# Performance work log

Measured on AMD Instinct MI355X. Metric: run time of the kernel, lower is better.

The kernel has to match this reference:

```python
import jax, jax.numpy as jnp
import numpy as np

HEADS = 8

def setup_inputs() -> dict:
    key = jax.random.key(0)
    ks = jax.random.split(key, 10)
    B, S, E = 2, 2048, 512
    q = jax.random.normal(ks[0], (B, S, E), jnp.float32)
    k = jax.random.normal(ks[1], (B, S, E), jnp.float32)
    v = jax.random.normal(ks[2], (B, S, E), jnp.float32)
    mask = jnp.zeros((S, S), jnp.float32)  # additive mask [s_q, s_k]
    scale = 0.02
    Wq = jax.random.normal(ks[3], (E, E), jnp.float32) * scale
    bq = jax.random.normal(ks[4], (E,), jnp.float32) * scale
    Wk = jax.random.normal(ks[5], (E, E), jnp.float32) * scale
    bk = jax.random.normal(ks[6], (E,), jnp.float32) * scale
    Wv = jax.random.normal(ks[7], (E, E), jnp.float32) * scale
    bv = jax.random.normal(ks[8], (E,), jnp.float32) * scale
    return {"q": q, "k": k, "v": v, "mask": mask,
            "Wq": Wq, "bq": bq, "Wk": Wk, "bk": bk, "Wv": Wv, "bv": bv}

def reference(q, k, v, mask, Wq, bq, Wk, bk, Wv, bv):
    H = HEADS
    b, s_q, _ = q.shape
    s_k = k.shape[1]
    s_v = v.shape[1]
    # NOTE: faithful to source: row-major view(b, H, s, -1) WITHOUT transposing
    # seq/head axes first (quirk of the original module).
    K = jnp.swapaxes((k @ Wk.T + bk).reshape(b, H, s_k, -1), 2, 3)  # [b,H,dh,s_k]
    Q = (q @ Wq.T + bq).reshape(b, H, s_q, -1)                      # [b,H,s_q,dh]
    V = (v @ Wv.T + bv).reshape(b, H, s_v, -1)                      # [b,H,s_v,dh]
    # NOTE: original scales by sqrt(K.shape[-1]) AFTER the transpose, i.e. sqrt(s_k)
    scores = (Q @ K) / jnp.sqrt(jnp.asarray(s_k, jnp.float32))      # [b,H,s_q,s_k]
    scores = scores + mask[:s_q, :s_k]
    attn = jax.nn.softmax(scores, axis=-1)
    out = (attn @ V).reshape(b, s_q, -1)  # [b, s_q, e]
    return out
```

## Files before the change

kernel.cpp:

```cpp
#include <hip/hip_runtime.h>


#define SEQ 2048
#define EMB 512
#define DH  64
#define MROWS 4096
#define NROWS 32768

typedef float  v4f __attribute__((ext_vector_type(4)));
typedef short  v8s __attribute__((ext_vector_type(8)));
typedef __fp16 v2h __attribute__((ext_vector_type(2)));

static __device__ __forceinline__ unsigned int f2bf(float f) {
    unsigned int u = __float_as_uint(f);
    u += 0x7fffu + ((u >> 16) & 1u);
    return u >> 16;
}
static __device__ __forceinline__ unsigned int pack2(float a, float b) {
    return f2bf(a) | (f2bf(b) << 16);
}
static __device__ __forceinline__ unsigned int packh2(float a, float b) {
    v2h h = __builtin_amdgcn_cvt_pkrtz(a, b);
    return __builtin_bit_cast(unsigned int, h);
}

__global__ __launch_bounds__(256, 3) void proj_kernel(
    const float* __restrict__ q, const float* __restrict__ k, const float* __restrict__ v,
    const float* __restrict__ Wq, const float* __restrict__ bq,
    const float* __restrict__ Wk, const float* __restrict__ bk,
    const float* __restrict__ Wv, const float* __restrict__ bv,
    const float* __restrict__ mask,
    unsigned short* __restrict__ Qbf, unsigned short* __restrict__ Kbf,
    unsigned short* __restrict__ Vbf, float* __restrict__ maskT,
    unsigned int* __restrict__ flags)
{
    __shared__ __align__(16) char smem[27648];
    const int tid = threadIdx.x;

    if (blockIdx.x >= 768) {
        const int mb2 = blockIdx.x - 768;
        const int rb = mb2 >> 5, kt = mb2 & 31;
        float* tile = maskT + ((size_t)rb * 32 + kt) * 8192;
        float4 vals[8];
        bool any = false;
#pragma unroll
        for (int i = 0; i < 8; ++i) {
            int s = tid + i * 256;
            int l  = s & 63;
            int cb = (s >> 6) & 3;
            int g  = (s >> 8) & 1;
            int w2 = (s >> 9) & 3;
            int qd2 = l >> 4, n2 = l & 15;
            vals[i] = *(const float4*)&mask[
                (size_t)(rb * 128 + w2 * 32 + g * 16 + n2) * SEQ + kt * 64 + cb * 16 + qd2 * 4];
            any = any | (vals[i].x != 0.f) | (vals[i].y != 0.f)
                      | (vals[i].z != 0.f) | (vals[i].w != 0.f);
        }
        unsigned int* nzp = (unsigned int*)smem;
        if (tid == 0) *nzp = 0u;
        __syncthreads();
        if (any) *nzp = 1u;
        __syncthreads();
        if (*nzp) {
#pragma unroll
            for (int i = 0; i < 8; ++i) {
                int s = tid + i * 256;
                *(float4*)&tile[(size_t)s * 4] = vals[i];
            }
            if (tid == 0) atomicOr(&flags[rb], 1u << kt);
        }
        return;
    }

    char* As = smem;
    char* Ws = smem + 9216;

    const int id  = blockIdx.x;
    const int pos = id & 31;
    const int nb  = pos >> 3;
    const int unit = (id >> 5) * 8 + (pos & 7);
    const int mb = unit & 63;
    const int z  = unit >> 6;

    const float* A    = (z == 0) ? q  : (z == 1) ? k  : v;
    const float* W    = (z == 0) ? Wq : (z == 1) ? Wk : Wv;
    const float* bias = (z == 0) ? bq : (z == 1) ? bk : bv;
    unsigned short* Cg = (z == 0) ? Qbf : (z == 1) ? Kbf : Vbf;

    const int w    = tid >> 6;
    const int lane = tid & 63;
    const int qd   = lane >> 4;
    const int n    = lane & 15;
    const int m0 = mb * 64, n0 = nb * 128;

    float4 areg[4], wreg[8];
#pragma unroll
    for (int i = 0; i < 4; ++i) {
        int c = tid + i * 256;
        areg[i] = *(const float4*)&A[(size_t)(m0 + (c >> 4)) * EMB + (c & 15) * 4];
    }
#pragma unroll
    for (int i = 0; i < 8; ++i) {
        int c = tid + i * 256;
        wreg[i] = *(const float4*)&W[(size_t)(n0 + (c >> 4)) * EMB + (c & 15) * 4];
    }

    v4f acc[8];
#pragma unroll
    for (int cb = 0; cb < 8; ++cb) acc[cb] = (v4f)0.f;

#pragma unroll 1
    for (int kt = 0; kt < 8; ++kt) {
        __syncthreads();
#pragma unroll
        for (int i = 0; i < 4; ++i) {
            int c = tid + i * 256;
            uint2 pk = { pack2(areg[i].x, areg[i].y), pack2(areg[i].z, areg[i].w) };
            *(uint2*)&As[(c >> 4) * 144 + (c & 15) * 8] = pk;
        }
#pragma unroll
        for (int i = 0; i < 8; ++i) {
            int c = tid + i * 256;
            uint2 pk = { pack2(wreg[i].x, wreg[i].y), pack2(wreg[i].z, wreg[i].w) };
            *(uint2*)&Ws[(c >> 4) * 144 + (c & 15) * 8] = pk;
        }
        __syncthreads();

        if (kt + 1 < 8) {
#pragma unroll
            for (int i = 0; i < 4; ++i) {
                int c = tid + i * 256;
                areg[i] = *(const float4*)&A[(size_t)(m0 + (c >> 4)) * EMB + (kt+1) * 64 + (c & 15) * 4];
            }
#pragma unroll
            for (int i = 0; i < 8; ++i) {
                int c = tid + i * 256;
                wreg[i] = *(const float4*)&W[(size_t)(n0 + (c >> 4)) * EMB + (kt+1) * 64 + (c & 15) * 4];
            }
        }

#pragma unroll
        for (int ks = 0; ks < 2; ++ks) {
            v8s af = *(const v8s*)&As[(w * 16 + n) * 144 + ks * 64 + qd * 16];
#pragma unroll
            for (int cb = 0; cb < 8; ++cb) {
                v8s bfr = *(const v8s*)&Ws[(cb * 16 + n) * 144 + ks * 64 + qd * 16];
                acc[cb] = __builtin_amdgcn_mfma_f32_16x16x32_bf16(af, bfr, acc[cb], 0, 0, 0);
            }
        }
    }

    const float osc = (z == 0) ? 0.02209708691207961f : 1.0f;
    float bb[8];
#pragma unroll
    for (int cb = 0; cb < 8; ++cb) bb[cb] = bias[n0 + cb * 16 + n];
#pragma unroll
    for (int cb = 0; cb < 8; ++cb)
#pragma unroll
        for (int r = 0; r < 4; ++r) acc[cb][r] = (acc[cb][r] + bb[cb]) * osc;

    __syncthreads();
    short* Ct = (short*)smem;
#pragma unroll
    for (int cb = 0; cb < 8; ++cb)
#pragma unroll
        for (int r = 0; r < 4; ++r)
            Ct[(w * 16 + qd * 4 + r) * 136 + cb * 16 + n] = (short)f2bf(acc[cb][r]);
    __syncthreads();
    const int rr = tid >> 2, q4 = tid & 3;
#pragma unroll
    for (int i = 0; i < 4; ++i) {
        uint4 t4 = *(const uint4*)&smem[rr * 272 + q4 * 64 + i * 16];
        *(uint4*)&Cg[(size_t)(m0 + rr) * EMB + n0 + q4 * 32 + i * 8] = t4;
    }
}

__global__ __launch_bounds__(256) void frag_kernel(
    const unsigned short* __restrict__ Kbf, const unsigned short* __restrict__ Vbf,
    unsigned short* __restrict__ Kfr, unsigned short* __restrict__ Vfr)
{
    __shared__ unsigned short T[64 * 136];
    const int bh = blockIdx.x, kt = blockIdx.y;
    const int tid = threadIdx.x;

    const unsigned short* Kh = Kbf + (size_t)bh * (SEQ * DH) + (size_t)kt * 64 * DH;
#pragma unroll
    for (int i = 0; i < 2; ++i) {
        int c = tid + i * 256;
        uint4 t4 = *(const uint4*)&Kh[c * 8];
        *(uint4*)&T[(c >> 3) * 136 + (c & 7) * 8] = t4;
    }
    __syncthreads();
    unsigned short* Ko = Kfr + ((size_t)bh * 32 + kt) * 4096;
#pragma unroll
    for (int i = 0; i < 2; ++i) {
        int idx = tid + i * 256;
        int f = idx >> 6, l = idx & 63;
        int ks = f >> 2, cb = f & 3, qd = l >> 4, n = l & 15;
        uint4 t4 = *(const uint4*)&T[(cb * 16 + n) * 136 + ks * 32 + qd * 8];
        *(uint4*)&Ko[idx * 8] = t4;
    }
    __syncthreads();
    const unsigned short* Vh = Vbf + (size_t)bh * (SEQ * DH) + (size_t)kt * 64 * DH;
#pragma unroll
    for (int i = 0; i < 2; ++i) {
        int c = tid + i * 256;
        int s_l = c >> 3, ch = c & 7;
        uint4 t4 = *(const uint4*)&Vh[c * 8];
        const unsigned short* e = (const unsigned short*)&t4;
#pragma unroll
        for (int j = 0; j < 8; ++j)
            T[(ch * 8 + j) * 136 + s_l] = e[j];
    }
    __syncthreads();
    unsigned short* Vo = Vfr + ((size_t)bh * 32 + kt) * 4096;
#pragma unroll
    for (int i = 0; i < 2; ++i) {
        int idx = tid + i * 256;
        int f = idx >> 6, l = idx & 63;
        int ks = f >> 2, cb = f & 3, qd = l >> 4, n = l & 15;
        uint4 t4 = *(const uint4*)&T[(cb * 16 + n) * 136 + ks * 32 + qd * 8];
        *(uint4*)&Vo[idx * 8] = t4;
    }
}

template <int SPLITS>
__global__ __launch_bounds__(256, 4) void attn_kernel(
    const unsigned short* __restrict__ Qbf,
    const unsigned short* __restrict__ Kfr, const unsigned short* __restrict__ Vfr,
    const float* __restrict__ maskT, const float* __restrict__ maskf,
    const unsigned int* __restrict__ flags,
    unsigned short* __restrict__ Opart, float* __restrict__ ml,
    float* __restrict__ out)
{
    __shared__ __align__(16) char smem[34816];
    const int tid  = threadIdx.x;
    const int w    = tid >> 6;
    const int lane = tid & 63;
    const int qd   = lane >> 4;
    const int n    = lane & 15;
    const int a_   = qd & 1;
    const bool diag = (a_ == (qd >> 1));

    const int id = blockIdx.x;
    const int bh = (id & 7) * 2 + ((id >> 3) & 1);
    const int unit = id >> 4;
    const int rb = unit & 15;
    const int kq = unit >> 4;
    const int KT0 = kq * (32 / SPLITS), KT1 = KT0 + 32 / SPLITS;

    const unsigned short* Qh  = Qbf + (size_t)bh * (SEQ * DH);
    const unsigned short* Kfh = Kfr + (size_t)bh * 32 * 4096;
    const unsigned short* Vfh = Vfr + (size_t)bh * 32 * 4096;

    const unsigned int fl = (SPLITS > 1) ? flags[rb] : 0u;

    v8s qf[2][2];
#pragma unroll
    for (int g = 0; g < 2; ++g) {
        const size_t qrow = (size_t)(rb * 128 + w * 32 + g * 16 + n);
#pragma unroll
        for (int ks = 0; ks < 2; ++ks)
            qf[g][ks] = *(const v8s*)&Qh[qrow * DH + ks * 32 + qd * 8];
    }

    float l_[2] = { 0.f, 0.f };
    v4f oacc[2][4];
#pragma unroll
    for (int g = 0; g < 2; ++g)
#pragma unroll
        for (int cb = 0; cb < 4; ++cb) oacc[g][cb] = (v4f)0.f;

#pragma unroll 1
    for (int kt = KT0; kt < KT1; ++kt) {
        const unsigned short* Kt = Kfh + (size_t)kt * 4096;
        const unsigned short* Vt = Vfh + (size_t)kt * 4096;

        v4f sacc[2][4];
        float4 mk[2][4];
        if (SPLITS > 1) {
            if (fl & (1u << kt)) {
                const float* tileF = maskT + ((size_t)rb * 32 + kt) * 8192;
#pragma unroll
                for (int g = 0; g < 2; ++g)
#pragma unroll
                    for (int cb = 0; cb < 4; ++cb)
                        sacc[g][cb] = *(const v4f*)&tileF[
                            (size_t)((((w * 2 + g) * 4 + cb) * 64) + qd * 16 + n) * 4];
            } else {
#pragma unroll
                for (int g = 0; g < 2; ++g)
#pragma unroll
                    for (int cb = 0; cb < 4; ++cb) sacc[g][cb] = (v4f)0.f;
            }
        } else {
#pragma unroll
            for (int g = 0; g < 2; ++g) {
                const size_t mrow = (size_t)(rb * 128 + w * 32 + g * 16 + n);
#pragma unroll
                for (int cb = 0; cb < 4; ++cb) {
                    mk[g][cb] = *(const float4*)&maskf[mrow * SEQ + kt * 64 + cb * 16 + qd * 4];
                    sacc[g][cb] = (v4f)0.f;
                }
            }
        }

#pragma unroll
        for (int ks = 0; ks < 2; ++ks)
#pragma unroll
            for (int cb = 0; cb < 4; ++cb) {
                v8s kf = *(const v8s*)&Kt[((ks * 4 + cb) * 64 + lane) * 8];
#pragma unroll
                for (int g = 0; g < 2; ++g)
                    sacc[g][cb] = __builtin_amdgcn_mfma_f32_16x16x32_bf16(kf, qf[g][ks], sacc[g][cb], 0, 0, 0);
            }

        v8s pfr[2][2];
#pragma unroll
        for (int g = 0; g < 2; ++g) {
            float rs = 0.f;
            unsigned int O_[4][2];
#pragma unroll
            for (int cb = 0; cb < 4; ++cb) {
                if (SPLITS == 1) {
                    sacc[g][cb][0] += mk[g][cb].x; sacc[g][cb][1] += mk[g][cb].y;
                    sacc[g][cb][2] += mk[g][cb].z; sacc[g][cb][3] += mk[g][cb].w;
                }
                float e0 = __expf(sacc[g][cb][0]);
                float e1 = __expf(sacc[g][cb][1]);
                float e2 = __expf(sacc[g][cb][2]);
                float e3 = __expf(sacc[g][cb][3]);
                rs += (e0 + e1) + (e2 + e3);
                O_[cb][0] = pack2(e0, e1);
                O_[cb][1] = pack2(e2, e3);
            }
            rs += __shfl_xor(rs, 16);
            rs += __shfl_xor(rs, 32);
            l_[g] += rs;
#pragma unroll
            for (int ks = 0; ks < 2; ++ks) {
                unsigned int t0 = a_ ? O_[2 * ks][0] : O_[2 * ks + 1][0];
                unsigned int t1 = a_ ? O_[2 * ks][1] : O_[2 * ks + 1][1];
                unsigned int r0 = __shfl_xor(t0, 16);
                unsigned int r1 = __shfl_xor(t1, 16);
                unsigned int Z00 = a_ ? r0 : O_[2 * ks][0];
                unsigned int Z01 = a_ ? r1 : O_[2 * ks][1];
                unsigned int Z10 = a_ ? O_[2 * ks + 1][0] : r0;
                unsigned int Z11 = a_ ? O_[2 * ks + 1][1] : r1;
                unsigned int s00 = __shfl_xor(Z00, 48);
                unsigned int s01 = __shfl_xor(Z01, 48);
                unsigned int s10 = __shfl_xor(Z10, 48);
                unsigned int s11 = __shfl_xor(Z11, 48);
                uint4 pw;
                pw.x = diag ? Z00 : s00;
                pw.y = diag ? Z01 : s01;
                pw.z = diag ? Z10 : s10;
                pw.w = diag ? Z11 : s11;
                pfr[g][ks] = __builtin_bit_cast(v8s, pw);
            }
        }

#pragma unroll
        for (int ks = 0; ks < 2; ++ks) {
#pragma unroll
            for (int cb = 0; cb < 4; ++cb) {
                v8s vf = *(const v8s*)&Vt[((ks * 4 + cb) * 64 + lane) * 8];
#pragma unroll
                for (int g = 0; g < 2; ++g)
                    oacc[g][cb] = __builtin_amdgcn_mfma_f32_16x16x32_bf16(vf, pfr[g][ks], oacc[g][cb], 0, 0, 0);
            }
        }
    }

    if (SPLITS == 1) {
#pragma unroll
        for (int g = 0; g < 2; ++g) {
            const float inv = 1.0f / l_[g];
#pragma unroll
            for (int cb = 0; cb < 4; ++cb)
#pragma unroll
                for (int r = 0; r < 4; ++r) oacc[g][cb][r] *= inv;
        }
    } else {
        if (qd == 0) {
#pragma unroll
            for (int g = 0; g < 2; ++g) {
                const size_t row = (size_t)bh * SEQ + rb * 128 + w * 32 + g * 16 + n;
                ml[(size_t)kq * NROWS + row] = l_[g];
            }
        }
    }
    __syncthreads();
#pragma unroll
    for (int g = 0; g < 2; ++g)
#pragma unroll
        for (int cb = 0; cb < 4; ++cb)
            *(v4f*)&smem[(w * 32 + g * 16 + n) * 272 + cb * 64 + qd * 16] = oacc[g][cb];
    __syncthreads();
    const int r_l = tid >> 1, hf = tid & 1;
    if (SPLITS == 1) {
        float* dst = &out[((size_t)bh * SEQ + rb * 128 + r_l) * DH + hf * 32];
#pragma unroll
        for (int i = 0; i < 8; ++i) {
            float4 t4 = *(const float4*)&smem[r_l * 272 + hf * 128 + i * 16];
            *(float4*)&dst[i * 4] = t4;
        }
    } else {
        unsigned short* dst = &Opart[((size_t)kq * NROWS + (size_t)bh * SEQ + rb * 128 + r_l) * DH + hf * 32];
#pragma unroll
        for (int i = 0; i < 4; ++i) {
            float4 f0 = *(const float4*)&smem[r_l * 272 + hf * 128 + i * 32];
            float4 f1 = *(const float4*)&smem[r_l * 272 + hf * 128 + i * 32 + 16];
            uint4 o = { packh2(f0.x, f0.y), packh2(f0.z, f0.w),
                        packh2(f1.x, f1.y), packh2(f1.z, f1.w) };
            *(uint4*)&dst[i * 8] = o;
        }
    }
}

__global__ __launch_bounds__(256) void combine_kernel(
    const unsigned int* __restrict__ Opart, const float* __restrict__ ml,
    float* __restrict__ out, int splits)
{
    const int tid = threadIdx.x;
    const size_t row = (size_t)blockIdx.x * 16 + (tid >> 4);
    const int d4 = (tid & 15) * 4;
    float denom = 0.f;
    float4 o = make_float4(0.f, 0.f, 0.f, 0.f);
    for (int s = 0; s < splits; ++s) {
        denom += ml[(size_t)s * NROWS + row];
        uint2 u = *(const uint2*)&Opart[((size_t)s * NROWS + row) * 32 + (d4 >> 1)];
        v2h h0 = __builtin_bit_cast(v2h, u.x);
        v2h h1 = __builtin_bit_cast(v2h, u.y);
        o.x += (float)h0.x; o.y += (float)h0.y;
        o.z += (float)h1.x; o.w += (float)h1.y;
    }
    const float inv = 1.0f / denom;
    o.x *= inv; o.y *= inv; o.z *= inv; o.w *= inv;
    *(float4*)&out[row * DH + d4] = o;
}

extern "C" void kernel_launch(void* const* d_in, const int* in_sizes, int n_in,
                              void* d_out, int out_size, void* d_ws, size_t ws_size,
                              hipStream_t stream) {
    const float* q    = (const float*)d_in[0];
    const float* k    = (const float*)d_in[1];
    const float* v    = (const float*)d_in[2];
    const float* mask = (const float*)d_in[3];
    const float* Wq   = (const float*)d_in[4];
    const float* bq   = (const float*)d_in[5];
    const float* Wk   = (const float*)d_in[6];
    const float* bk   = (const float*)d_in[7];
    const float* Wv   = (const float*)d_in[8];
    const float* bv   = (const float*)d_in[9];

    char* ws = (char*)d_ws;
    const size_t MB = 1024 * 1024;
    unsigned short* Qbf   = (unsigned short*)(ws + 0);
    unsigned short* Kbf   = (unsigned short*)(ws + 4 * MB);
    unsigned short* Vfr   = (unsigned short*)(ws + 8 * MB);
    unsigned short* Opart = (unsigned short*)(ws + 12 * MB);
    unsigned short* Vbf   = (unsigned short*)(ws + 12 * MB);
    float*          mlp   = (float*)(ws + 28 * MB);
    unsigned int*   flags = (unsigned int*)(ws + 28 * MB + 512 * 1024);
    float*          maskT = (float*)(ws + 29 * MB);

    const size_t need_split = 49 * MB;
    const bool do_split = ws_size >= need_split;

    if (do_split) {
        unsigned short* Kfr = (unsigned short*)(ws + 45 * MB);
        (void)hipMemsetAsync(flags, 0, 64, stream);
        proj_kernel<<<1280, 256, 0, stream>>>(q, k, v, Wq, bq, Wk, bk, Wv, bv,
                                              mask, Qbf, Kbf, Vbf, maskT, flags);
        dim3 tgrid(16, 32);
        frag_kernel<<<tgrid, 256, 0, stream>>>(Kbf, Vbf, Kfr, Vfr);
        attn_kernel<4><<<1024, 256, 0, stream>>>(Qbf, Kfr, Vfr, maskT, mask, flags,
                                                 Opart, mlp, (float*)d_out);
        combine_kernel<<<NROWS / 16, 256, 0, stream>>>((const unsigned int*)Opart,
                                                       mlp, (float*)d_out, 4);
    } else {
        unsigned short* Kfr = (unsigned short*)(ws + 16 * MB);
        proj_kernel<<<768, 256, 0, stream>>>(q, k, v, Wq, bq, Wk, bk, Wv, bv,
                                             mask, Qbf, Kbf, Vbf, maskT, flags);
        dim3 tgrid(16, 32);
        frag_kernel<<<tgrid, 256, 0, stream>>>(Kbf, Vbf, Kfr, Vfr);
        attn_kernel<1><<<256, 256, 0, stream>>>(Qbf, Kfr, Vfr, maskT, mask, flags,
                                                Opart, mlp, (float*)d_out);
    }
}
```

Baseline: 172.4 us.

## Prefetch next K tile into registers and switch softmax to exp2 with hardware bf16 pack

The attention loop now double-buffers K fragments in registers, loading tile kt+1 while computing tile kt, with the loop unrolled by two so the buffers swap without copies. The Q scale and mask values are pre-multiplied by log2(e) so exp can use the native exp2 instruction. Software bf16 rounding is replaced by the hardware v_cvt_pk_bf16_f32 instruction. This costs extra VGPRs for the second K buffer and assumes an even tile count per split.

```diff
diff --git a/kernel.cpp b/kernel.cpp
--- a/kernel.cpp
+++ b/kernel.cpp
@@ -6,6 +6,7 @@
 #define DH  64
 #define MROWS 4096
 #define NROWS 32768
+#define L2E 1.4426950408889634f
 
 typedef float  v4f __attribute__((ext_vector_type(4)));
 typedef short  v8s __attribute__((ext_vector_type(8)));
@@ -65,6 +66,8 @@
 #pragma unroll
             for (int i = 0; i < 8; ++i) {
                 int s = tid + i * 256;
+                vals[i].x *= L2E; vals[i].y *= L2E;
+                vals[i].z *= L2E; vals[i].w *= L2E;
                 *(float4*)&tile[(size_t)s * 4] = vals[i];
             }
             if (tid == 0) atomicOr(&flags[rb], 1u << kt);
@@ -150,7 +153,7 @@
         }
     }
 
-    const float osc = (z == 0) ? 0.02209708691207961f : 1.0f;
+    const float osc = (z == 0) ? 0.031879357905f : 1.0f;
     float bb[8];
 #pragma unroll
     for (int cb = 0; cb < 8; ++cb) bb[cb] = bias[n0 + cb * 16 + n];
@@ -249,9 +252,9 @@
     const int kq = unit >> 4;
     const int KT0 = kq * (32 / SPLITS), KT1 = KT0 + 32 / SPLITS;
 
-    const unsigned short* Qh  = Qbf + (size_t)bh * (SEQ * DH);
-    const unsigned short* Kfh = Kfr + (size_t)bh * 32 * 4096;
-    const unsigned short* Vfh = Vfr + (size_t)bh * 32 * 4096;
+    const unsigned short* Qh = Qbf + (size_t)bh * (SEQ * DH);
+    const unsigned short* KL = Kfr + (size_t)bh * 32 * 4096 + lane * 8;
+    const unsigned short* VL = Vfr + (size_t)bh * 32 * 4096 + lane * 8;
 
     const unsigned int fl = (SPLITS > 1) ? flags[rb] : 0u;
 
@@ -271,10 +274,17 @@
 #pragma unroll
         for (int cb = 0; cb < 4; ++cb) oacc[g][cb] = (v4f)0.f;
 
-#pragma unroll 1
-    for (int kt = KT0; kt < KT1; ++kt) {
-        const unsigned short* Kt = Kfh + (size_t)kt * 4096;
-        const unsigned short* Vt = Vfh + (size_t)kt * 4096;
+    v8s ka[8], kb[8];
+#pragma unroll
+    for (int f = 0; f < 8; ++f)
+        ka[f] = *(const v8s*)&KL[(size_t)KT0 * 4096 + f * 512];
+
+    auto step = [&](int kt, v8s (&KC)[8], v8s (&KN)[8], bool dopf) {
+        if (dopf) {
+#pragma unroll
+            for (int f = 0; f < 8; ++f)
+                KN[f] = *(const v8s*)&KL[(size_t)(kt + 1) * 4096 + f * 512];
+        }
 
         v4f sacc[2][4];
         float4 mk[2][4];
@@ -308,12 +318,11 @@
 #pragma unroll
         for (int ks = 0; ks < 2; ++ks)
 #pragma unroll
-            for (int cb = 0; cb < 4; ++cb) {
-                v8s kf = *(const v8s*)&Kt[((ks * 4 + cb) * 64 + lane) * 8];
+            for (int cb = 0; cb < 4; ++cb)
 #pragma unroll
                 for (int g = 0; g < 2; ++g)
-                    sacc[g][cb] = __builtin_amdgcn_mfma_f32_16x16x32_bf16(kf, qf[g][ks], sacc[g][cb], 0, 0, 0);
-            }
+                    sacc[g][cb] = __builtin_amdgcn_mfma_f32_16x16x32_bf16(
+                        KC[ks * 4 + cb], qf[g][ks], sacc[g][cb], 0, 0, 0);
 
         v8s pfr[2][2];
 #pragma unroll
@@ -322,17 +331,21 @@
             unsigned int O_[4][2];
 #pragma unroll
             for (int cb = 0; cb < 4; ++cb) {
+                float s0 = sacc[g][cb][0], s1 = sacc[g][cb][1];
+                float s2 = sacc[g][cb][2], s3 = sacc[g][cb][3];
                 if (SPLITS == 1) {
-                    sacc[g][cb][0] += mk[g][cb].x; sacc[g][cb][1] += mk[g][cb].y;
-                    sacc[g][cb][2] += mk[g][cb].z; sacc[g][cb][3] += mk[g][cb].w;
+                    s0 = fmaf(mk[g][cb].x, L2E, s0);
+                    s1 = fmaf(mk[g][cb].y, L2E, s1);
+                    s2 = fmaf(mk[g][cb].z, L2E, s2);
+                    s3 = fmaf(mk[g][cb].w, L2E, s3);
                 }
-                float e0 = __expf(sacc[g][cb][0]);
-                float e1 = __expf(sacc[g][cb][1]);
-                float e2 = __expf(sacc[g][cb][2]);
-                float e3 = __expf(sacc[g][cb][3]);
+                float e0 = __builtin_amdgcn_exp2f(s0);
+                float e1 = __builtin_amdgcn_exp2f(s1);
+                float e2 = __builtin_amdgcn_exp2f(s2);
+                float e3 = __builtin_amdgcn_exp2f(s3);
                 rs += (e0 + e1) + (e2 + e3);
-                O_[cb][0] = pack2(e0, e1);
-                O_[cb][1] = pack2(e2, e3);
+                asm("v_cvt_pk_bf16_f32 %0, %1, %2" : "=v"(O_[cb][0]) : "v"(e0), "v"(e1));
+                asm("v_cvt_pk_bf16_f32 %0, %1, %2" : "=v"(O_[cb][1]) : "v"(e2), "v"(e3));
             }
             rs += __shfl_xor(rs, 16);
             rs += __shfl_xor(rs, 32);
@@ -361,15 +374,21 @@
         }
 
 #pragma unroll
-        for (int ks = 0; ks < 2; ++ks) {
+        for (int ks = 0; ks < 2; ++ks)
 #pragma unroll
             for (int cb = 0; cb < 4; ++cb) {
-                v8s vf = *(const v8s*)&Vt[((ks * 4 + cb) * 64 + lane) * 8];
+                v8s vf = *(const v8s*)&VL[(size_t)kt * 4096 + (ks * 4 + cb) * 512];
 #pragma unroll
                 for (int g = 0; g < 2; ++g)
-                    oacc[g][cb] = __builtin_amdgcn_mfma_f32_16x16x32_bf16(vf, pfr[g][ks], oacc[g][cb], 0, 0, 0);
-            }
-        }
+                    oacc[g][cb] = __builtin_amdgcn_mfma_f32_16x16x32_bf16(
+                        vf, pfr[g][ks], oacc[g][cb], 0, 0, 0);
+            }
+    };
+
+#pragma unroll 1
+    for (int kt2 = KT0; kt2 < KT1; kt2 += 2) {
+        step(kt2,     ka, kb, true);
+        step(kt2 + 1, kb, ka, kt2 + 2 < KT1);
     }
 
     if (SPLITS == 1) {
```

New measurement: 199.4 us. 1.16x slower.

## Halve attention row block to 64 rows and switch softmax to exp2

Applied to the files above, without the earlier changes.

The attention kernel now processes 64 query rows per block (16 per wave) instead of 128, doubling the grid and cutting registers and shared memory so the launch bound rises to 6 blocks per CU. Separately, log2(e) is folded into the Q scale and the mask tile, so the softmax uses the native exp2 instruction instead of __expf. Each K/V fragment load now feeds half as many MFMAs, so global and L2 traffic for K/V per unit of work doubles, in exchange for higher occupancy and better latency hiding.

```diff
diff --git a/kernel.cpp b/kernel.cpp
--- a/kernel.cpp
+++ b/kernel.cpp
@@ -6,6 +6,7 @@
 #define DH  64
 #define MROWS 4096
 #define NROWS 32768
+#define L2E 1.4426950408889634f
 
 typedef float  v4f __attribute__((ext_vector_type(4)));
 typedef short  v8s __attribute__((ext_vector_type(8)));
@@ -65,6 +66,8 @@
 #pragma unroll
             for (int i = 0; i < 8; ++i) {
                 int s = tid + i * 256;
+                vals[i].x *= L2E; vals[i].y *= L2E;
+                vals[i].z *= L2E; vals[i].w *= L2E;
                 *(float4*)&tile[(size_t)s * 4] = vals[i];
             }
             if (tid == 0) atomicOr(&flags[rb], 1u << kt);
@@ -150,7 +153,7 @@
         }
     }
 
-    const float osc = (z == 0) ? 0.02209708691207961f : 1.0f;
+    const float osc = (z == 0) ? 0.031879357905f : 1.0f;
     float bb[8];
 #pragma unroll
     for (int cb = 0; cb < 8; ++cb) bb[cb] = bias[n0 + cb * 16 + n];
@@ -225,7 +228,7 @@
 }
 
 template <int SPLITS>
-__global__ __launch_bounds__(256, 4) void attn_kernel(
+__global__ __launch_bounds__(256, 6) void attn_kernel(
     const unsigned short* __restrict__ Qbf,
     const unsigned short* __restrict__ Kfr, const unsigned short* __restrict__ Vfr,
     const float* __restrict__ maskT, const float* __restrict__ maskf,
@@ -233,7 +236,7 @@
     unsigned short* __restrict__ Opart, float* __restrict__ ml,
     float* __restrict__ out)
 {
-    __shared__ __align__(16) char smem[34816];
+    __shared__ __align__(16) char smem[17408];
     const int tid  = threadIdx.x;
     const int w    = tid >> 6;
     const int lane = tid & 63;
@@ -245,63 +248,54 @@
     const int id = blockIdx.x;
     const int bh = (id & 7) * 2 + ((id >> 3) & 1);
     const int unit = id >> 4;
-    const int rb = unit & 15;
-    const int kq = unit >> 4;
+    const int rb6 = unit & 31;
+    const int kq = unit >> 5;
     const int KT0 = kq * (32 / SPLITS), KT1 = KT0 + 32 / SPLITS;
 
     const unsigned short* Qh  = Qbf + (size_t)bh * (SEQ * DH);
     const unsigned short* Kfh = Kfr + (size_t)bh * 32 * 4096;
     const unsigned short* Vfh = Vfr + (size_t)bh * 32 * 4096;
 
-    const unsigned int fl = (SPLITS > 1) ? flags[rb] : 0u;
-
-    v8s qf[2][2];
-#pragma unroll
-    for (int g = 0; g < 2; ++g) {
-        const size_t qrow = (size_t)(rb * 128 + w * 32 + g * 16 + n);
+    const unsigned int fl = (SPLITS > 1) ? flags[rb6 >> 1] : 0u;
+
+    v8s qf[2];
+    {
+        const size_t qrow = (size_t)(rb6 * 64 + w * 16 + n);
 #pragma unroll
         for (int ks = 0; ks < 2; ++ks)
-            qf[g][ks] = *(const v8s*)&Qh[qrow * DH + ks * 32 + qd * 8];
-    }
-
-    float l_[2] = { 0.f, 0.f };
-    v4f oacc[2][4];
-#pragma unroll
-    for (int g = 0; g < 2; ++g)
-#pragma unroll
-        for (int cb = 0; cb < 4; ++cb) oacc[g][cb] = (v4f)0.f;
+            qf[ks] = *(const v8s*)&Qh[qrow * DH + ks * 32 + qd * 8];
+    }
+
+    float l_ = 0.f;
+    v4f oacc[4];
+#pragma unroll
+    for (int cb = 0; cb < 4; ++cb) oacc[cb] = (v4f)0.f;
 
 #pragma unroll 1
     for (int kt = KT0; kt < KT1; ++kt) {
         const unsigned short* Kt = Kfh + (size_t)kt * 4096;
         const unsigned short* Vt = Vfh + (size_t)kt * 4096;
 
-        v4f sacc[2][4];
-        float4 mk[2][4];
+        v4f sacc[4];
+        float4 mk[4];
         if (SPLITS > 1) {
             if (fl & (1u << kt)) {
-                const float* tileF = maskT + ((size_t)rb * 32 + kt) * 8192;
-#pragma unroll
-                for (int g = 0; g < 2; ++g)
-#pragma unroll
-                    for (int cb = 0; cb < 4; ++cb)
-                        sacc[g][cb] = *(const v4f*)&tileF[
-                            (size_t)((((w * 2 + g) * 4 + cb) * 64) + qd * 16 + n) * 4];
+                const float* tileF = maskT + ((size_t)(rb6 >> 1) * 32 + kt) * 8192;
+                const int wg = (rb6 & 1) * 4 + w;
+#pragma unroll
+                for (int cb = 0; cb < 4; ++cb)
+                    sacc[cb] = *(const v4f*)&tileF[
+                        (size_t)((wg * 4 + cb) * 64 + qd * 16 + n) * 4];
             } else {
 #pragma unroll
-                for (int g = 0; g < 2; ++g)
-#pragma unroll
-                    for (int cb = 0; cb < 4; ++cb) sacc[g][cb] = (v4f)0.f;
+                for (int cb = 0; cb < 4; ++cb) sacc[cb] = (v4f)0.f;
             }
         } else {
-#pragma unroll
-            for (int g = 0; g < 2; ++g) {
-                const size_t mrow = (size_t)(rb * 128 + w * 32 + g * 16 + n);
-#pragma unroll
-                for (int cb = 0; cb < 4; ++cb) {
-                    mk[g][cb] = *(const float4*)&maskf[mrow * SEQ + kt * 64 + cb * 16 + qd * 4];
-                    sacc[g][cb] = (v4f)0.f;
-                }
+            const size_t mrow = (size_t)(rb6 * 64 + w * 16 + n);
+#pragma unroll
+            for (int cb = 0; cb < 4; ++cb) {
+                mk[cb] = *(const float4*)&maskf[mrow * SEQ + kt * 64 + cb * 16 + qd * 4];
+                sacc[cb] = (v4f)0.f;
             }
         }
 
@@ -310,33 +304,34 @@
 #pragma unroll
             for (int cb = 0; cb < 4; ++cb) {
                 v8s kf = *(const v8s*)&Kt[((ks * 4 + cb) * 64 + lane) * 8];
-#pragma unroll
-                for (int g = 0; g < 2; ++g)
-                    sacc[g][cb] = __builtin_amdgcn_mfma_f32_16x16x32_bf16(kf, qf[g][ks], sacc[g][cb], 0, 0, 0);
-            }
-
-        v8s pfr[2][2];
-#pragma unroll
-        for (int g = 0; g < 2; ++g) {
+                sacc[cb] = __builtin_amdgcn_mfma_f32_16x16x32_bf16(kf, qf[ks], sacc[cb], 0, 0, 0);
+            }
+
+        v8s pfr[2];
+        {
             float rs = 0.f;
             unsigned int O_[4][2];
 #pragma unroll
             for (int cb = 0; cb < 4; ++cb) {
+                float s0 = sacc[cb][0], s1 = sacc[cb][1];
+                float s2 = sacc[cb][2], s3 = sacc[cb][3];
                 if (SPLITS == 1) {
-                    sacc[g][cb][0] += mk[g][cb].x; sacc[g][cb][1] += mk[g][cb].y;
-                    sacc[g][cb][2] += mk[g][cb].z; sacc[g][cb][3] += mk[g][cb].w;
+                    s0 = fmaf(mk[cb].x, L2E, s0);
+                    s1 = fmaf(mk[cb].y, L2E, s1);
+                    s2 = fmaf(mk[cb].z, L2E, s2);
+                    s3 = fmaf(mk[cb].w, L2E, s3);
                 }
-                float e0 = __expf(sacc[g][cb][0]);
-                float e1 = __expf(sacc[g][cb][1]);
-                float e2 = __expf(sacc[g][cb][2]);
-                float e3 = __expf(sacc[g][cb][3]);
+                float e0 = __builtin_amdgcn_exp2f(s0);
+                float e1 = __builtin_amdgcn_exp2f(s1);
+                float e2 = __builtin_amdgcn_exp2f(s2);
+                float e3 = __builtin_amdgcn_exp2f(s3);
                 rs += (e0 + e1) + (e2 + e3);
                 O_[cb][0] = pack2(e0, e1);
                 O_[cb][1] = pack2(e2, e3);
             }
             rs += __shfl_xor(rs, 16);
             rs += __shfl_xor(rs, 32);
-            l_[g] += rs;
+            l_ += rs;
 #pragma unroll
             for (int ks = 0; ks < 2; ++ks) {
                 unsigned int t0 = a_ ? O_[2 * ks][0] : O_[2 * ks + 1][0];
@@ -356,61 +351,50 @@
                 pw.y = diag ? Z01 : s01;
                 pw.z = diag ? Z10 : s10;
                 pw.w = diag ? Z11 : s11;
-                pfr[g][ks] = __builtin_bit_cast(v8s, pw);
-            }
-        }
-
-#pragma unroll
-        for (int ks = 0; ks < 2; ++ks) {
+                pfr[ks] = __builtin_bit_cast(v8s, pw);
+            }
+        }
+
+#pragma unroll
+        for (int ks = 0; ks < 2; ++ks)
 #pragma unroll
             for (int cb = 0; cb < 4; ++cb) {
                 v8s vf = *(const v8s*)&Vt[((ks * 4 + cb) * 64 + lane) * 8];
-#pragma unroll
-                for (int g = 0; g < 2; ++g)
-                    oacc[g][cb] = __builtin_amdgcn_mfma_f32_16x16x32_bf16(vf, pfr[g][ks], oacc[g][cb], 0, 0, 0);
-            }
-        }
+                oacc[cb] = __builtin_amdgcn_mfma_f32_16x16x32_bf16(vf, pfr[ks], oacc[cb], 0, 0, 0);
+            }
     }
 
     if (SPLITS == 1) {
-#pragma unroll
-        for (int g = 0; g < 2; ++g) {
-            const float inv = 1.0f / l_[g];
-#pragma unroll
-            for (int cb = 0; cb < 4; ++cb)
-#pragma unroll
-                for (int r = 0; r < 4; ++r) oacc[g][cb][r] *= inv;
-        }
+        const float inv = 1.0f / l_;
+#pragma unroll
+        for (int cb = 0; cb < 4; ++cb)
+#pragma unroll
+            for (int r = 0; r < 4; ++r) oacc[cb][r] *= inv;
     } else {
         if (qd == 0) {
-#pragma unroll
-            for (int g = 0; g < 2; ++g) {
-                const size_t row = (size_t)bh * SEQ + rb * 128 + w * 32 + g * 16 + n;
-                ml[(size_t)kq * NROWS + row] = l_[g];
-            }
-        }
-    }
-    __syncthreads();
-#pragma unroll
-    for (int g = 0; g < 2; ++g)
-#pragma unroll
-        for (int cb = 0; cb < 4; ++cb)
-            *(v4f*)&smem[(w * 32 + g * 16 + n) * 272 + cb * 64 + qd * 16] = oacc[g][cb];
-    __syncthreads();
-    const int r_l = tid >> 1, hf = tid & 1;
+            const size_t row = (size_t)bh * SEQ + rb6 * 64 + w * 16 + n;
+            ml[(size_t)kq * NROWS + row] = l_;
+        }
+    }
+    __syncthreads();
+#pragma unroll
+    for (int cb = 0; cb < 4; ++cb)
+        *(v4f*)&smem[(w * 16 + n) * 272 + cb * 64 + qd * 16] = oacc[cb];
+    __syncthreads();
+    const int r_l = tid >> 2, q4 = tid & 3;
     if (SPLITS == 1) {
-        float* dst = &out[((size_t)bh * SEQ + rb * 128 + r_l) * DH + hf * 32];
-#pragma unroll
-        for (int i = 0; i < 8; ++i) {
-            float4 t4 = *(const float4*)&smem[r_l * 272 + hf * 128 + i * 16];
+        float* dst = &out[((size_t)bh * SEQ + rb6 * 64 + r_l) * DH + q4 * 16];
+#pragma unroll
+        for (int i = 0; i < 4; ++i) {
+            float4 t4 = *(const float4*)&smem[r_l * 272 + q4 * 64 + i * 16];
             *(float4*)&dst[i * 4] = t4;
         }
     } else {
-        unsigned short* dst = &Opart[((size_t)kq * NROWS + (size_t)bh * SEQ + rb * 128 + r_l) * DH + hf * 32];
-#pragma unroll
-        for (int i = 0; i < 4; ++i) {
-            float4 f0 = *(const float4*)&smem[r_l * 272 + hf * 128 + i * 32];
-            float4 f1 = *(const float4*)&smem[r_l * 272 + hf * 128 + i * 32 + 16];
+        unsigned short* dst = &Opart[((size_t)kq * NROWS + (size_t)bh * SEQ + rb6 * 64 + r_l) * DH + q4 * 16];
+#pragma unroll
+        for (int i = 0; i < 2; ++i) {
+            float4 f0 = *(const float4*)&smem[r_l * 272 + q4 * 64 + i * 32];
+            float4 f1 = *(const float4*)&smem[r_l * 272 + q4 * 64 + i * 32 + 16];
             uint4 o = { packh2(f0.x, f0.y), packh2(f0.z, f0.w),
                         packh2(f1.x, f1.y), packh2(f1.z, f1.w) };
             *(uint4*)&dst[i * 8] = o;
@@ -475,7 +459,7 @@
                                               mask, Qbf, Kbf, Vbf, maskT, flags);
         dim3 tgrid(16, 32);
         frag_kernel<<<tgrid, 256, 0, stream>>>(Kbf, Vbf, Kfr, Vfr);
-        attn_kernel<4><<<1024, 256, 0, stream>>>(Qbf, Kfr, Vfr, maskT, mask, flags,
+        attn_kernel<4><<<2048, 256, 0, stream>>>(Qbf, Kfr, Vfr, maskT, mask, flags,
                                                  Opart, mlp, (float*)d_out);
         combine_kernel<<<NROWS / 16, 256, 0, stream>>>((const unsigned int*)Opart,
                                                        mlp, (float*)d_out, 4);
@@ -485,7 +469,7 @@
                                              mask, Qbf, Kbf, Vbf, maskT, flags);
         dim3 tgrid(16, 32);
         frag_kernel<<<tgrid, 256, 0, stream>>>(Kbf, Vbf, Kfr, Vfr);
-        attn_kernel<1><<<256, 256, 0, stream>>>(Qbf, Kfr, Vfr, maskT, mask, flags,
+        attn_kernel<1><<<512, 256, 0, stream>>>(Qbf, Kfr, Vfr, maskT, mask, flags,
                                                 Opart, mlp, (float*)d_out);
     }
 }
```

Result: no change. 173.1 us (+0.4%).
